# Kernel optimization log

Hardware: AMD Instinct MI355X
Metric: run time of the kernel (lower is better)

The kernel has to match this reference:

```python
import jax, jax.numpy as jnp
import numpy as np

B, N, K_NB, C, KERNEL, OUT = 32, 128, 16, 1024, 8, 1024
TWO_PI = 2.0 * np.pi
EPS = 1e-14


def setup_inputs() -> dict:
    key = jax.random.key(0)
    ks = jax.random.split(key, 9)
    return {
        "node_feats": jax.random.normal(ks[0], (B, N, C), dtype=jnp.float32),
        "node_centre": jax.random.uniform(ks[1], (B, N, 2), dtype=jnp.float32),
        "neighbor_idx": jax.random.randint(ks[2], (B, N, K_NB), 0, N, dtype=jnp.int32),
        "graph_weights": jax.random.uniform(ks[3], (B, N, K_NB), dtype=jnp.float32),
        "mean_rho": jax.random.uniform(ks[4], (1, KERNEL), dtype=jnp.float32),
        "mean_theta": jax.random.uniform(ks[5], (1, KERNEL), minval=-np.pi, maxval=np.pi, dtype=jnp.float32),
        "precision_rho": jax.random.uniform(ks[6], (1, KERNEL), dtype=jnp.float32),
        "precision_theta": jax.random.uniform(ks[7], (1, KERNEL), dtype=jnp.float32),
        "conv_w": jax.random.normal(ks[8], (KERNEL, C, OUT // KERNEL), dtype=jnp.float32) * 0.02,
    }


def _gaussian_weights(node_centre, neighbor_idx, mean_rho, mean_theta, precision_rho, precision_theta):
    # gather neighbor centres per batch: [B,N,K,2]
    centre_j = jax.vmap(lambda c, idx: c[idx])(node_centre, neighbor_idx)
    diff = node_centre[:, :, None, :] - centre_j           # node_i - node_j
    cx, cy = diff[..., 0], diff[..., 1]                    # chunk order: x first
    rho = jnp.sqrt(cx ** 2 + cy ** 2)                      # [B,N,K]
    theta = jnp.arctan2(cx, cy)                            # note: atan2(x, y) as in source
    d_rho = (rho[..., None] - mean_rho[0]) ** 2            # [B,N,K,KERNEL]
    w_rho = jnp.exp(-0.5 * d_rho / (EPS + precision_rho[0] ** 2))
    a1 = jnp.abs(theta[..., None] - mean_theta[0])
    a2 = jnp.abs(TWO_PI - a1)
    w_theta = jnp.exp(-0.5 * jnp.minimum(a1, a2) ** 2 / (EPS + precision_theta[0] ** 2))
    w = w_rho * w_theta
    w = jnp.where(jnp.isnan(w), 0.0, w)
    return w / jnp.sum(w, axis=-1, keepdims=True)          # normalize over kernel dim


def reference(node_feats, node_centre, neighbor_idx, graph_weights,
              mean_rho, mean_theta, precision_rho, precision_theta, conv_w):
    gw = _gaussian_weights(node_centre, neighbor_idx, mean_rho, mean_theta,
                           precision_rho, precision_theta)       # [B,N,K,KERNEL]
    edge_w = graph_weights[..., None] * gw                        # use_graph_weights=True
    # gather neighbor features per batch: [B,N,K,C]
    feats_j = jax.vmap(lambda f, idx: f[idx])(node_feats, neighbor_idx)
    # bmm aggregation: [B,N,KERNEL,C]
    agg = jnp.einsum('bnkm,bnkc->bnmc', edge_w, feats_j)
    # per-kernel linear (no bias) then concat: [B,N,KERNEL,OUT//KERNEL] -> [B,N,OUT]
    out = jnp.einsum('bnmc,mcd->bnmd', agg, conv_w)
    out = out.reshape(node_feats.shape[0], node_feats.shape[1], -1)
    return jax.nn.relu(out)
```

## Files before the change

kernel.cpp:

```cpp
#include <hip/hip_runtime.h>
#include <hip/hip_bf16.h>

#define B_   32
#define N_   128
#define KNB  16
#define C_   1024
#define KER  8
#define DOUT 128
#define OUTC 1024
#define BN_TOT (B_ * N_)
#define BK   64
#define NT   (C_ / BK)

typedef __attribute__((ext_vector_type(8))) short bf16x8;
typedef __attribute__((ext_vector_type(4))) float f32x4;

__device__ __forceinline__ ushort f2bf(float f) {
    unsigned u = __builtin_bit_cast(unsigned, f);
    unsigned r = (u + 0x7FFFu + ((u >> 16) & 1u)) >> 16;
    return (ushort)r;
}

#define GLOAD_LDS16(gp, lp)                                                    \
    __builtin_amdgcn_global_load_lds(                                          \
        (__attribute__((address_space(1))) void*)(gp),                         \
        (__attribute__((address_space(3))) void*)(lp), 16, 0, 0)

__global__ __launch_bounds__(256) void k_convert_f(const float* __restrict__ f,
                                                   ushort* __restrict__ Fb) {
    int t = blockIdx.x * 256 + threadIdx.x;
    float4 v = ((const float4*)f)[t];
    ushort4 o;
    o.x = f2bf(v.x); o.y = f2bf(v.y); o.z = f2bf(v.z); o.w = f2bf(v.w);
    ((ushort4*)Fb)[t] = o;
}

__global__ __launch_bounds__(256) void k_transpose_w(const float* __restrict__ cw,
                                                     ushort* __restrict__ WbT) {
    __shared__ float tile[32][33];
    int bid = blockIdx.x;
    int dt = bid & 3;
    int ct = (bid >> 2) & 31;
    int m  = bid >> 7;
    int tx = threadIdx.x & 31;
    int ty = threadIdx.x >> 5;
#pragma unroll
    for (int i = 0; i < 4; ++i) {
        int cr = ty + i * 8;
        tile[cr][tx] = cw[((size_t)m * C_ + (ct * 32 + cr)) * DOUT + dt * 32 + tx];
    }
    __syncthreads();
#pragma unroll
    for (int i = 0; i < 4; ++i) {
        int dr = ty + i * 8;
        WbT[((size_t)(m * DOUT + dt * 32 + dr)) * C_ + ct * 32 + tx] = f2bf(tile[tx][dr]);
    }
}

__global__ __launch_bounds__(256) void k_edgew(const float* __restrict__ centre,
                                               const int* __restrict__ nidx,
                                               const float* __restrict__ gw,
                                               const float* __restrict__ mr,
                                               const float* __restrict__ mt,
                                               const float* __restrict__ pr,
                                               const float* __restrict__ pt,
                                               float* __restrict__ ew) {
    int t = blockIdx.x * 256 + threadIdx.x;
    int bn = t >> 4;
    int b  = bn >> 7;
    float2 ci = *(const float2*)(centre + (size_t)bn * 2);
    int j = nidx[t];
    float2 cj = *(const float2*)(centre + (size_t)(b * N_ + j) * 2);
    float cx = ci.x - cj.x, cy = ci.y - cj.y;
    float rho = sqrtf(cx * cx + cy * cy);
    float theta = atan2f(cx, cy);
    float w[KER];
    float sum = 0.f;
#pragma unroll
    for (int m = 0; m < KER; ++m) {
        float dr = rho - mr[m];
        float wr = expf(-0.5f * dr * dr / (1e-14f + pr[m] * pr[m]));
        float a1 = fabsf(theta - mt[m]);
        float a2 = fabsf(6.2831853071795864f - a1);
        float am = fminf(a1, a2);
        float wt = expf(-0.5f * am * am / (1e-14f + pt[m] * pt[m]));
        float wv = wr * wt;
        if (isnan(wv)) wv = 0.f;
        w[m] = wv;
        sum += wv;
    }
    float scale = gw[t] / sum;
#pragma unroll
    for (int m = 0; m < KER; ++m) ew[(size_t)t * KER + m] = w[m] * scale;
}

__global__ __launch_bounds__(512) void k_gemm_fused(const ushort* __restrict__ Fb,
                                                    const ushort* __restrict__ WbT,
                                                    const float* __restrict__ ew,
                                                    const int* __restrict__ nidx,
                                                    float* __restrict__ out) {
    __shared__ __align__(16) char smem[67584];

    int tid  = threadIdx.x;
    int wave = tid >> 6;
    int lane = tid & 63;
    int wm = wave >> 2;
    int wn = wave & 3;
    int lr = lane & 15;
    int kg = lane >> 4;
    int b = blockIdx.x;
    int m = blockIdx.y;

    const ushort* Abase = Fb  + (size_t)b * N_ * C_;
    const ushort* Bbase = WbT + (size_t)m * DOUT * C_;

    f32x4 acc[4][2];
#pragma unroll
    for (int i = 0; i < 4; ++i)
#pragma unroll
        for (int j = 0; j < 2; ++j) acc[i][j] = (f32x4){0.f, 0.f, 0.f, 0.f};

    auto STAGE = [&](int buf, int kt) {
        ushort* As = (ushort*)(smem + buf * 32768);
        ushort* Bs = (ushort*)(smem + buf * 32768 + 16384);
#pragma unroll
        for (int i = 0; i < 2; ++i) {
            int segb = i * 512 + wave * 64;
            int seg  = segb + lane;
            int row  = seg >> 3;
            int ch   = (seg & 7) ^ (row & 7);
            const ushort* ga = Abase + (size_t)row * C_ + kt * BK + ch * 8;
            GLOAD_LDS16(ga, As + segb * 8);
            const ushort* gb = Bbase + (size_t)row * C_ + kt * BK + ch * 8;
            GLOAD_LDS16(gb, Bs + segb * 8);
        }
    };

    int aoff[4][2], boff[2][2];
#pragma unroll
    for (int mi = 0; mi < 4; ++mi)
#pragma unroll
        for (int kk = 0; kk < 2; ++kk) {
            int row = wm * 64 + mi * 16 + lr;
            int ch  = (kk * 4 + kg) ^ (row & 7);
            aoff[mi][kk] = row * 128 + ch * 16;
        }
#pragma unroll
    for (int ni = 0; ni < 2; ++ni)
#pragma unroll
        for (int kk = 0; kk < 2; ++kk) {
            int row = wn * 32 + ni * 16 + lr;
            int ch  = (kk * 4 + kg) ^ (row & 7);
            boff[ni][kk] = 16384 + row * 128 + ch * 16;
        }

    STAGE(0, 0);
    for (int kt = 0; kt < NT; ++kt) {
        int cur = kt & 1;
        const char* bufp = smem + cur * 32768;
        if (kt + 1 < NT) {
            STAGE(cur ^ 1, kt + 1);
            asm volatile("s_waitcnt vmcnt(4)" ::: "memory");
        } else {
            asm volatile("s_waitcnt vmcnt(0)" ::: "memory");
        }
        __builtin_amdgcn_s_barrier();
#pragma unroll
        for (int kk = 0; kk < 2; ++kk) {
            bf16x8 af[4], bv[2];
#pragma unroll
            for (int mi = 0; mi < 4; ++mi)
                af[mi] = *(const bf16x8*)(bufp + aoff[mi][kk]);
#pragma unroll
            for (int ni = 0; ni < 2; ++ni)
                bv[ni] = *(const bf16x8*)(bufp + boff[ni][kk]);
#pragma unroll
            for (int mi = 0; mi < 4; ++mi)
#pragma unroll
                for (int ni = 0; ni < 2; ++ni)
                    acc[mi][ni] = __builtin_amdgcn_mfma_f32_16x16x32_bf16(
                        af[mi], bv[ni], acc[mi][ni], 0, 0, 0);
        }
        asm volatile("" ::: "memory");
        __builtin_amdgcn_s_barrier();
    }

    float* Gt = (float*)smem;
#pragma unroll
    for (int mi = 0; mi < 4; ++mi)
#pragma unroll
        for (int ni = 0; ni < 2; ++ni)
#pragma unroll
            for (int r = 0; r < 4; ++r) {
                int grow = wm * 64 + mi * 16 + kg * 4 + r;
                int gcol = wn * 32 + ni * 16 + lr;
                Gt[grow * 132 + gcol] = acc[mi][ni][r];
            }
    __syncthreads();

    int n = tid >> 2, q = tid & 3;
    const int*   ip = nidx + (size_t)(b * N_ + n) * KNB;
    const float* ep = ew   + (size_t)(b * N_ + n) * (KNB * KER) + m;
    f32x4 o[8];
#pragma unroll
    for (int i = 0; i < 8; ++i) o[i] = (f32x4){0.f, 0.f, 0.f, 0.f};
#pragma unroll
    for (int k = 0; k < KNB; ++k) {
        int j = ip[k];
        float w = ep[k * KER];
        const float* gr = Gt + j * 132 + q * 32;
#pragma unroll
        for (int i = 0; i < 8; ++i) {
            f32x4 v = *(const f32x4*)(gr + i * 4);
            o[i] += v * w;
        }
    }
    float* op = out + (size_t)(b * N_ + n) * OUTC + m * DOUT + q * 32;
#pragma unroll
    for (int i = 0; i < 8; ++i) {
        f32x4 r = o[i];
#pragma unroll
        for (int jj = 0; jj < 4; ++jj) r[jj] = fmaxf(r[jj], 0.f);
        *(f32x4*)(op + i * 4) = r;
    }
}

extern "C" void kernel_launch(void* const* d_in, const int* in_sizes, int n_in,
                              void* d_out, int out_size, void* d_ws, size_t ws_size,
                              hipStream_t stream) {
    const float* node_feats      = (const float*)d_in[0];
    const float* node_centre     = (const float*)d_in[1];
    const int*   neighbor_idx    = (const int*)d_in[2];
    const float* graph_weights   = (const float*)d_in[3];
    const float* mean_rho        = (const float*)d_in[4];
    const float* mean_theta      = (const float*)d_in[5];
    const float* precision_rho   = (const float*)d_in[6];
    const float* precision_theta = (const float*)d_in[7];
    const float* conv_w          = (const float*)d_in[8];
    float* out = (float*)d_out;

    char* ws = (char*)d_ws;
    ushort* Fb  = (ushort*)(ws);
    ushort* WbT = (ushort*)(ws + (8u  << 20));
    float*  ew  = (float*) (ws + (10u << 20));

    k_convert_f  <<<4096, 256, 0, stream>>>(node_feats, Fb);
    k_transpose_w<<<1024, 256, 0, stream>>>(conv_w, WbT);
    k_edgew      <<<256, 256, 0, stream>>>(node_centre, neighbor_idx, graph_weights,
                                           mean_rho, mean_theta,
                                           precision_rho, precision_theta, ew);
    dim3 ggrid(B_, KER);
    k_gemm_fused <<<ggrid, 512, 0, stream>>>(Fb, WbT, ew, neighbor_idx, out);
}
```

Baseline: 113.2 us.

## Merge prep kernels, triple-buffer GEMM loads, rotate epilogue LDS access order

Combines the three preprocessing kernels into one launch dispatched by block index, to remove launch overhead and tail gaps. The GEMM main loop moves from double to triple buffering in LDS, staging two tiles ahead with matching vmcnt waits, to hide global load latency better. The epilogue rotates the column chunk order per lane group to reduce LDS bank conflicts on the gather reads. LDS use grows to 96KB per block, which limits residency.

After: 110.1 us. -2.8%, faster.

```diff
diff --git a/kernel.cpp b/kernel.cpp
--- a/kernel.cpp
+++ b/kernel.cpp
@@ -26,72 +26,74 @@
         (__attribute__((address_space(1))) void*)(gp),                         \
         (__attribute__((address_space(3))) void*)(lp), 16, 0, 0)
 
-__global__ __launch_bounds__(256) void k_convert_f(const float* __restrict__ f,
-                                                   ushort* __restrict__ Fb) {
-    int t = blockIdx.x * 256 + threadIdx.x;
-    float4 v = ((const float4*)f)[t];
-    ushort4 o;
-    o.x = f2bf(v.x); o.y = f2bf(v.y); o.z = f2bf(v.z); o.w = f2bf(v.w);
-    ((ushort4*)Fb)[t] = o;
-}
-
-__global__ __launch_bounds__(256) void k_transpose_w(const float* __restrict__ cw,
-                                                     ushort* __restrict__ WbT) {
+__global__ __launch_bounds__(256) void k_prep(const float* __restrict__ f,
+                                              ushort* __restrict__ Fb,
+                                              const float* __restrict__ cw,
+                                              ushort* __restrict__ WbT,
+                                              const float* __restrict__ centre,
+                                              const int* __restrict__ nidx,
+                                              const float* __restrict__ gw,
+                                              const float* __restrict__ mr,
+                                              const float* __restrict__ mt,
+                                              const float* __restrict__ pr,
+                                              const float* __restrict__ pt,
+                                              float* __restrict__ ew) {
     __shared__ float tile[32][33];
     int bid = blockIdx.x;
-    int dt = bid & 3;
-    int ct = (bid >> 2) & 31;
-    int m  = bid >> 7;
-    int tx = threadIdx.x & 31;
-    int ty = threadIdx.x >> 5;
-#pragma unroll
-    for (int i = 0; i < 4; ++i) {
-        int cr = ty + i * 8;
-        tile[cr][tx] = cw[((size_t)m * C_ + (ct * 32 + cr)) * DOUT + dt * 32 + tx];
-    }
-    __syncthreads();
-#pragma unroll
-    for (int i = 0; i < 4; ++i) {
-        int dr = ty + i * 8;
-        WbT[((size_t)(m * DOUT + dt * 32 + dr)) * C_ + ct * 32 + tx] = f2bf(tile[tx][dr]);
-    }
-}
-
-__global__ __launch_bounds__(256) void k_edgew(const float* __restrict__ centre,
-                                               const int* __restrict__ nidx,
-                                               const float* __restrict__ gw,
-                                               const float* __restrict__ mr,
-                                               const float* __restrict__ mt,
-                                               const float* __restrict__ pr,
-                                               const float* __restrict__ pt,
-                                               float* __restrict__ ew) {
-    int t = blockIdx.x * 256 + threadIdx.x;
-    int bn = t >> 4;
-    int b  = bn >> 7;
-    float2 ci = *(const float2*)(centre + (size_t)bn * 2);
-    int j = nidx[t];
-    float2 cj = *(const float2*)(centre + (size_t)(b * N_ + j) * 2);
-    float cx = ci.x - cj.x, cy = ci.y - cj.y;
-    float rho = sqrtf(cx * cx + cy * cy);
-    float theta = atan2f(cx, cy);
-    float w[KER];
-    float sum = 0.f;
-#pragma unroll
-    for (int m = 0; m < KER; ++m) {
-        float dr = rho - mr[m];
-        float wr = expf(-0.5f * dr * dr / (1e-14f + pr[m] * pr[m]));
-        float a1 = fabsf(theta - mt[m]);
-        float a2 = fabsf(6.2831853071795864f - a1);
-        float am = fminf(a1, a2);
-        float wt = expf(-0.5f * am * am / (1e-14f + pt[m] * pt[m]));
-        float wv = wr * wt;
-        if (isnan(wv)) wv = 0.f;
-        w[m] = wv;
-        sum += wv;
-    }
-    float scale = gw[t] / sum;
-#pragma unroll
-    for (int m = 0; m < KER; ++m) ew[(size_t)t * KER + m] = w[m] * scale;
+    int tid = threadIdx.x;
+    if (bid < 4096) {
+        int t = bid * 256 + tid;
+        float4 v = ((const float4*)f)[t];
+        ushort4 o;
+        o.x = f2bf(v.x); o.y = f2bf(v.y); o.z = f2bf(v.z); o.w = f2bf(v.w);
+        ((ushort4*)Fb)[t] = o;
+    } else if (bid < 5120) {
+        int b2 = bid - 4096;
+        int dt = b2 & 3;
+        int ct = (b2 >> 2) & 31;
+        int m  = b2 >> 7;
+        int tx = tid & 31;
+        int ty = tid >> 5;
+#pragma unroll
+        for (int i = 0; i < 4; ++i) {
+            int cr = ty + i * 8;
+            tile[cr][tx] = cw[((size_t)m * C_ + (ct * 32 + cr)) * DOUT + dt * 32 + tx];
+        }
+        __syncthreads();
+#pragma unroll
+        for (int i = 0; i < 4; ++i) {
+            int dr = ty + i * 8;
+            WbT[((size_t)(m * DOUT + dt * 32 + dr)) * C_ + ct * 32 + tx] = f2bf(tile[tx][dr]);
+        }
+    } else {
+        int t = (bid - 5120) * 256 + tid;
+        int bn = t >> 4;
+        int b  = bn >> 7;
+        float2 ci = *(const float2*)(centre + (size_t)bn * 2);
+        int j = nidx[t];
+        float2 cj = *(const float2*)(centre + (size_t)(b * N_ + j) * 2);
+        float cx = ci.x - cj.x, cy = ci.y - cj.y;
+        float rho = sqrtf(cx * cx + cy * cy);
+        float theta = atan2f(cx, cy);
+        float w[KER];
+        float sum = 0.f;
+#pragma unroll
+        for (int m = 0; m < KER; ++m) {
+            float dr = rho - mr[m];
+            float wr = expf(-0.5f * dr * dr / (1e-14f + pr[m] * pr[m]));
+            float a1 = fabsf(theta - mt[m]);
+            float a2 = fabsf(6.2831853071795864f - a1);
+            float am = fminf(a1, a2);
+            float wt = expf(-0.5f * am * am / (1e-14f + pt[m] * pt[m]));
+            float wv = wr * wt;
+            if (isnan(wv)) wv = 0.f;
+            w[m] = wv;
+            sum += wv;
+        }
+        float scale = gw[t] / sum;
+#pragma unroll
+        for (int m = 0; m < KER; ++m) ew[(size_t)t * KER + m] = w[m] * scale;
+    }
 }
 
 __global__ __launch_bounds__(512) void k_gemm_fused(const ushort* __restrict__ Fb,
@@ -99,7 +101,7 @@
                                                     const float* __restrict__ ew,
                                                     const int* __restrict__ nidx,
                                                     float* __restrict__ out) {
-    __shared__ __align__(16) char smem[67584];
+    __shared__ __align__(16) char smem[98304];
 
     int tid  = threadIdx.x;
     int wave = tid >> 6;
@@ -155,11 +157,14 @@
         }
 
     STAGE(0, 0);
+    STAGE(1, 1);
     for (int kt = 0; kt < NT; ++kt) {
-        int cur = kt & 1;
+        int cur = kt % 3;
         const char* bufp = smem + cur * 32768;
-        if (kt + 1 < NT) {
-            STAGE(cur ^ 1, kt + 1);
+        if (kt + 2 < NT) {
+            STAGE((kt + 2) % 3, kt + 2);
+            asm volatile("s_waitcnt vmcnt(8)" ::: "memory");
+        } else if (kt + 1 < NT) {
             asm volatile("s_waitcnt vmcnt(4)" ::: "memory");
         } else {
             asm volatile("s_waitcnt vmcnt(0)" ::: "memory");
@@ -201,6 +206,9 @@
     int n = tid >> 2, q = tid & 3;
     const int*   ip = nidx + (size_t)(b * N_ + n) * KNB;
     const float* ep = ew   + (size_t)(b * N_ + n) * (KNB * KER) + m;
+    int rot[8];
+#pragma unroll
+    for (int i = 0; i < 8; ++i) rot[i] = (q * 4 + i * 4) & 31;
     f32x4 o[8];
 #pragma unroll
     for (int i = 0; i < 8; ++i) o[i] = (f32x4){0.f, 0.f, 0.f, 0.f};
@@ -211,7 +219,7 @@
         const float* gr = Gt + j * 132 + q * 32;
 #pragma unroll
         for (int i = 0; i < 8; ++i) {
-            f32x4 v = *(const f32x4*)(gr + i * 4);
+            f32x4 v = *(const f32x4*)(gr + rot[i]);
             o[i] += v * w;
         }
     }
@@ -221,7 +229,7 @@
         f32x4 r = o[i];
 #pragma unroll
         for (int jj = 0; jj < 4; ++jj) r[jj] = fmaxf(r[jj], 0.f);
-        *(f32x4*)(op + i * 4) = r;
+        *(f32x4*)(op + rot[i]) = r;
     }
 }
 
@@ -244,11 +252,10 @@
     ushort* WbT = (ushort*)(ws + (8u  << 20));
     float*  ew  = (float*) (ws + (10u << 20));
 
-    k_convert_f  <<<4096, 256, 0, stream>>>(node_feats, Fb);
-    k_transpose_w<<<1024, 256, 0, stream>>>(conv_w, WbT);
-    k_edgew      <<<256, 256, 0, stream>>>(node_centre, neighbor_idx, graph_weights,
-                                           mean_rho, mean_theta,
-                                           precision_rho, precision_theta, ew);
+    k_prep<<<5376, 256, 0, stream>>>(node_feats, Fb, conv_w, WbT,
+                                     node_centre, neighbor_idx, graph_weights,
+                                     mean_rho, mean_theta,
+                                     precision_rho, precision_theta, ew);
     dim3 ggrid(B_, KER);
-    k_gemm_fused <<<ggrid, 512, 0, stream>>>(Fb, WbT, ew, neighbor_idx, out);
-}
+    k_gemm_fused<<<ggrid, 512, 0, stream>>>(Fb, WbT, ew, neighbor_idx, out);
+}
```

## Fuse fp32-to-bf16 feature conversion into GEMM and merge prep kernels

Applied to the files above, without the earlier changes.

Removes the standalone feature conversion kernel. The GEMM now loads fp32 node features into registers, converts them to bf16 and writes them to swizzled LDS, software-pipelined two tiles ahead, while the weight tile still uses direct global-to-LDS loads. The weight transpose and edge-weight kernels are merged into one launch, which cuts launch count and avoids the bf16 feature round trip through memory. The gather epilogue also rotates its column order per quad to spread LDS bank accesses. The tradeoffs are more register pressure, VALU conversion work inside the main loop, and eight-fold redundant fp32 feature reads across the m blocks.

New measurement: 109.1 us. 3.6% less time.

```diff
diff --git a/kernel.cpp b/kernel.cpp
--- a/kernel.cpp
+++ b/kernel.cpp
@@ -8,7 +8,6 @@
 #define KER  8
 #define DOUT 128
 #define OUTC 1024
-#define BN_TOT (B_ * N_)
 #define BK   64
 #define NT   (C_ / BK)
 
@@ -26,79 +25,72 @@
         (__attribute__((address_space(1))) void*)(gp),                         \
         (__attribute__((address_space(3))) void*)(lp), 16, 0, 0)
 
-__global__ __launch_bounds__(256) void k_convert_f(const float* __restrict__ f,
-                                                   ushort* __restrict__ Fb) {
-    int t = blockIdx.x * 256 + threadIdx.x;
-    float4 v = ((const float4*)f)[t];
-    ushort4 o;
-    o.x = f2bf(v.x); o.y = f2bf(v.y); o.z = f2bf(v.z); o.w = f2bf(v.w);
-    ((ushort4*)Fb)[t] = o;
-}
-
-__global__ __launch_bounds__(256) void k_transpose_w(const float* __restrict__ cw,
-                                                     ushort* __restrict__ WbT) {
+__global__ __launch_bounds__(256) void k_prep(const float* __restrict__ cw,
+                                              ushort* __restrict__ WbT,
+                                              const float* __restrict__ centre,
+                                              const int* __restrict__ nidx,
+                                              const float* __restrict__ gw,
+                                              const float* __restrict__ mr,
+                                              const float* __restrict__ mt,
+                                              const float* __restrict__ pr,
+                                              const float* __restrict__ pt,
+                                              float* __restrict__ ew) {
     __shared__ float tile[32][33];
     int bid = blockIdx.x;
-    int dt = bid & 3;
-    int ct = (bid >> 2) & 31;
-    int m  = bid >> 7;
-    int tx = threadIdx.x & 31;
-    int ty = threadIdx.x >> 5;
-#pragma unroll
-    for (int i = 0; i < 4; ++i) {
-        int cr = ty + i * 8;
-        tile[cr][tx] = cw[((size_t)m * C_ + (ct * 32 + cr)) * DOUT + dt * 32 + tx];
-    }
-    __syncthreads();
-#pragma unroll
-    for (int i = 0; i < 4; ++i) {
-        int dr = ty + i * 8;
-        WbT[((size_t)(m * DOUT + dt * 32 + dr)) * C_ + ct * 32 + tx] = f2bf(tile[tx][dr]);
-    }
-}
-
-__global__ __launch_bounds__(256) void k_edgew(const float* __restrict__ centre,
+    int tid = threadIdx.x;
+    if (bid < 1024) {
+        int dt = bid & 3;
+        int ct = (bid >> 2) & 31;
+        int m  = bid >> 7;
+        int tx = tid & 31;
+        int ty = tid >> 5;
+#pragma unroll
+        for (int i = 0; i < 4; ++i) {
+            int cr = ty + i * 8;
+            tile[cr][tx] = cw[((size_t)m * C_ + (ct * 32 + cr)) * DOUT + dt * 32 + tx];
+        }
+        __syncthreads();
+#pragma unroll
+        for (int i = 0; i < 4; ++i) {
+            int dr = ty + i * 8;
+            WbT[((size_t)(m * DOUT + dt * 32 + dr)) * C_ + ct * 32 + tx] = f2bf(tile[tx][dr]);
+        }
+    } else {
+        int t = (bid - 1024) * 256 + tid;
+        int bn = t >> 4;
+        int b  = bn >> 7;
+        float2 ci = *(const float2*)(centre + (size_t)bn * 2);
+        int j = nidx[t];
+        float2 cj = *(const float2*)(centre + (size_t)(b * N_ + j) * 2);
+        float cx = ci.x - cj.x, cy = ci.y - cj.y;
+        float rho = sqrtf(cx * cx + cy * cy);
+        float theta = atan2f(cx, cy);
+        float w[KER];
+        float sum = 0.f;
+#pragma unroll
+        for (int m = 0; m < KER; ++m) {
+            float dr = rho - mr[m];
+            float wr = expf(-0.5f * dr * dr / (1e-14f + pr[m] * pr[m]));
+            float a1 = fabsf(theta - mt[m]);
+            float a2 = fabsf(6.2831853071795864f - a1);
+            float am = fminf(a1, a2);
+            float wt = expf(-0.5f * am * am / (1e-14f + pt[m] * pt[m]));
+            float wv = wr * wt;
+            if (isnan(wv)) wv = 0.f;
+            w[m] = wv;
+            sum += wv;
+        }
+        float scale = gw[t] / sum;
+#pragma unroll
+        for (int m = 0; m < KER; ++m) ew[(size_t)t * KER + m] = w[m] * scale;
+    }
+}
+
+__global__ __launch_bounds__(512) void k_fused(const float* __restrict__ F,
+                                               const ushort* __restrict__ WbT,
+                                               const float* __restrict__ ew,
                                                const int* __restrict__ nidx,
-                                               const float* __restrict__ gw,
-                                               const float* __restrict__ mr,
-                                               const float* __restrict__ mt,
-                                               const float* __restrict__ pr,
-                                               const float* __restrict__ pt,
-                                               float* __restrict__ ew) {
-    int t = blockIdx.x * 256 + threadIdx.x;
-    int bn = t >> 4;
-    int b  = bn >> 7;
-    float2 ci = *(const float2*)(centre + (size_t)bn * 2);
-    int j = nidx[t];
-    float2 cj = *(const float2*)(centre + (size_t)(b * N_ + j) * 2);
-    float cx = ci.x - cj.x, cy = ci.y - cj.y;
-    float rho = sqrtf(cx * cx + cy * cy);
-    float theta = atan2f(cx, cy);
-    float w[KER];
-    float sum = 0.f;
-#pragma unroll
-    for (int m = 0; m < KER; ++m) {
-        float dr = rho - mr[m];
-        float wr = expf(-0.5f * dr * dr / (1e-14f + pr[m] * pr[m]));
-        float a1 = fabsf(theta - mt[m]);
-        float a2 = fabsf(6.2831853071795864f - a1);
-        float am = fminf(a1, a2);
-        float wt = expf(-0.5f * am * am / (1e-14f + pt[m] * pt[m]));
-        float wv = wr * wt;
-        if (isnan(wv)) wv = 0.f;
-        w[m] = wv;
-        sum += wv;
-    }
-    float scale = gw[t] / sum;
-#pragma unroll
-    for (int m = 0; m < KER; ++m) ew[(size_t)t * KER + m] = w[m] * scale;
-}
-
-__global__ __launch_bounds__(512) void k_gemm_fused(const ushort* __restrict__ Fb,
-                                                    const ushort* __restrict__ WbT,
-                                                    const float* __restrict__ ew,
-                                                    const int* __restrict__ nidx,
-                                                    float* __restrict__ out) {
+                                               float* __restrict__ out) {
     __shared__ __align__(16) char smem[67584];
 
     int tid  = threadIdx.x;
@@ -111,8 +103,13 @@
     int b = blockIdx.x;
     int m = blockIdx.y;
 
-    const ushort* Abase = Fb  + (size_t)b * N_ * C_;
-    const ushort* Bbase = WbT + (size_t)m * DOUT * C_;
+    const float*  Af = F   + (size_t)b * N_ * C_;
+    const ushort* Bb = WbT + (size_t)m * DOUT * C_;
+
+    int arow = tid >> 2, qq = tid & 3;
+    const float* asrc = Af + (size_t)arow * C_ + qq * 16;
+    int as0 = ((qq * 2)     ^ (arow & 7)) * 8 + arow * 64;
+    int as1 = ((qq * 2 + 1) ^ (arow & 7)) * 8 + arow * 64;
 
     f32x4 acc[4][2];
 #pragma unroll
@@ -120,8 +117,46 @@
 #pragma unroll
         for (int j = 0; j < 2; ++j) acc[i][j] = (f32x4){0.f, 0.f, 0.f, 0.f};
 
-    auto STAGE = [&](int buf, int kt) {
+    f32x4 areg[4];
+
+    int aoff[4][2], boff[2][2];
+#pragma unroll
+    for (int mi = 0; mi < 4; ++mi)
+#pragma unroll
+        for (int kk = 0; kk < 2; ++kk) {
+            int row = wm * 64 + mi * 16 + lr;
+            int ch  = (kk * 4 + kg) ^ (row & 7);
+            aoff[mi][kk] = row * 128 + ch * 16;
+        }
+#pragma unroll
+    for (int ni = 0; ni < 2; ++ni)
+#pragma unroll
+        for (int kk = 0; kk < 2; ++kk) {
+            int row = wn * 32 + ni * 16 + lr;
+            int ch  = (kk * 4 + kg) ^ (row & 7);
+            boff[ni][kk] = 16384 + row * 128 + ch * 16;
+        }
+
+    auto A_ISSUE = [&](int kt) {
+#pragma unroll
+        for (int i = 0; i < 4; ++i)
+            areg[i] = *(const f32x4*)(asrc + kt * BK + i * 4);
+    };
+    auto A_WRITE = [&](int buf) {
         ushort* As = (ushort*)(smem + buf * 32768);
+        bf16x8 w0, w1;
+#pragma unroll
+        for (int i = 0; i < 2; ++i)
+#pragma unroll
+            for (int j = 0; j < 4; ++j) w0[i * 4 + j] = (short)f2bf(areg[i][j]);
+#pragma unroll
+        for (int i = 0; i < 2; ++i)
+#pragma unroll
+            for (int j = 0; j < 4; ++j) w1[i * 4 + j] = (short)f2bf(areg[2 + i][j]);
+        *(bf16x8*)(As + as0) = w0;
+        *(bf16x8*)(As + as1) = w1;
+    };
+    auto B_ISSUE = [&](int buf, int kt) {
         ushort* Bs = (ushort*)(smem + buf * 32768 + 16384);
 #pragma unroll
         for (int i = 0; i < 2; ++i) {
@@ -129,42 +164,28 @@
             int seg  = segb + lane;
             int row  = seg >> 3;
             int ch   = (seg & 7) ^ (row & 7);
-            const ushort* ga = Abase + (size_t)row * C_ + kt * BK + ch * 8;
-            GLOAD_LDS16(ga, As + segb * 8);
-            const ushort* gb = Bbase + (size_t)row * C_ + kt * BK + ch * 8;
+            const ushort* gb = Bb + (size_t)row * C_ + kt * BK + ch * 8;
             GLOAD_LDS16(gb, Bs + segb * 8);
         }
     };
 
-    int aoff[4][2], boff[2][2];
-#pragma unroll
-    for (int mi = 0; mi < 4; ++mi)
-#pragma unroll
-        for (int kk = 0; kk < 2; ++kk) {
-            int row = wm * 64 + mi * 16 + lr;
-            int ch  = (kk * 4 + kg) ^ (row & 7);
-            aoff[mi][kk] = row * 128 + ch * 16;
-        }
-#pragma unroll
-    for (int ni = 0; ni < 2; ++ni)
-#pragma unroll
-        for (int kk = 0; kk < 2; ++kk) {
-            int row = wn * 32 + ni * 16 + lr;
-            int ch  = (kk * 4 + kg) ^ (row & 7);
-            boff[ni][kk] = 16384 + row * 128 + ch * 16;
-        }
-
-    STAGE(0, 0);
+    A_ISSUE(0);
+    B_ISSUE(0, 0);
+    A_WRITE(0);
+    A_ISSUE(1);
+    asm volatile("s_waitcnt vmcnt(4)" ::: "memory");
+    asm volatile("s_waitcnt lgkmcnt(0)" ::: "memory");
+    __builtin_amdgcn_s_barrier();
+
     for (int kt = 0; kt < NT; ++kt) {
         int cur = kt & 1;
         const char* bufp = smem + cur * 32768;
         if (kt + 1 < NT) {
-            STAGE(cur ^ 1, kt + 1);
-            asm volatile("s_waitcnt vmcnt(4)" ::: "memory");
-        } else {
-            asm volatile("s_waitcnt vmcnt(0)" ::: "memory");
-        }
-        __builtin_amdgcn_s_barrier();
+            A_WRITE(cur ^ 1);
+            B_ISSUE(cur ^ 1, kt + 1);
+        }
+        if (kt + 2 < NT) A_ISSUE(kt + 2);
+
 #pragma unroll
         for (int kk = 0; kk < 2; ++kk) {
             bf16x8 af[4], bv[2];
@@ -181,10 +202,18 @@
                     acc[mi][ni] = __builtin_amdgcn_mfma_f32_16x16x32_bf16(
                         af[mi], bv[ni], acc[mi][ni], 0, 0, 0);
         }
-        asm volatile("" ::: "memory");
-        __builtin_amdgcn_s_barrier();
-    }
-
+
+        if (kt + 1 < NT) {
+            if (kt + 2 < NT)
+                asm volatile("s_waitcnt vmcnt(4)" ::: "memory");
+            else
+                asm volatile("s_waitcnt vmcnt(0)" ::: "memory");
+            asm volatile("s_waitcnt lgkmcnt(0)" ::: "memory");
+            __builtin_amdgcn_s_barrier();
+        }
+    }
+
+    __syncthreads();
     float* Gt = (float*)smem;
 #pragma unroll
     for (int mi = 0; mi < 4; ++mi)
@@ -201,6 +230,9 @@
     int n = tid >> 2, q = tid & 3;
     const int*   ip = nidx + (size_t)(b * N_ + n) * KNB;
     const float* ep = ew   + (size_t)(b * N_ + n) * (KNB * KER) + m;
+    int rot[8];
+#pragma unroll
+    for (int i = 0; i < 8; ++i) rot[i] = (q * 4 + i * 4) & 31;
     f32x4 o[8];
 #pragma unroll
     for (int i = 0; i < 8; ++i) o[i] = (f32x4){0.f, 0.f, 0.f, 0.f};
@@ -211,7 +243,7 @@
         const float* gr = Gt + j * 132 + q * 32;
 #pragma unroll
         for (int i = 0; i < 8; ++i) {
-            f32x4 v = *(const f32x4*)(gr + i * 4);
+            f32x4 v = *(const f32x4*)(gr + rot[i]);
             o[i] += v * w;
         }
     }
@@ -221,7 +253,7 @@
         f32x4 r = o[i];
 #pragma unroll
         for (int jj = 0; jj < 4; ++jj) r[jj] = fmaxf(r[jj], 0.f);
-        *(f32x4*)(op + i * 4) = r;
+        *(f32x4*)(op + rot[i]) = r;
     }
 }
 
@@ -240,15 +272,13 @@
     float* out = (float*)d_out;
 
     char* ws = (char*)d_ws;
-    ushort* Fb  = (ushort*)(ws);
-    ushort* WbT = (ushort*)(ws + (8u  << 20));
-    float*  ew  = (float*) (ws + (10u << 20));
-
-    k_convert_f  <<<4096, 256, 0, stream>>>(node_feats, Fb);
-    k_transpose_w<<<1024, 256, 0, stream>>>(conv_w, WbT);
-    k_edgew      <<<256, 256, 0, stream>>>(node_centre, neighbor_idx, graph_weights,
-                                           mean_rho, mean_theta,
-                                           precision_rho, precision_theta, ew);
+    ushort* WbT = (ushort*)(ws);
+    float*  ew  = (float*) (ws + (2u << 20));
+
+    k_prep<<<1280, 256, 0, stream>>>(conv_w, WbT,
+                                     node_centre, neighbor_idx, graph_weights,
+                                     mean_rho, mean_theta,
+                                     precision_rho, precision_theta, ew);
     dim3 ggrid(B_, KER);
-    k_gemm_fused <<<ggrid, 512, 0, stream>>>(Fb, WbT, ew, neighbor_idx, out);
-}
+    k_fused<<<ggrid, 512, 0, stream>>>(node_feats, WbT, ew, neighbor_idx, out);
+}
```
